# Optimization experiments

Hardware: AMD Instinct MI355X
Metric: run time of the kernel (lower is better)

The kernel has to match this reference:

```python
import jax, jax.numpy as jnp
import numpy as np

GAM1 = 1.0
GAM2 = 1.0
EPS = 0.01


def setup_inputs() -> dict:
    key = jax.random.key(0)
    kx, ky = jax.random.split(key)
    m, p, k = 16384, 512, 10
    X = jax.random.normal(kx, (m, p), dtype=jnp.float32)
    Y = jax.random.randint(ky, (m,), 0, k, dtype=jnp.int64)
    return {"X": X, "Y": Y, "num_classes": k}


def reference(X, Y, num_classes):
    # W: [p, m] (features x samples), as in the torch module (W = X.T)
    W = X.reshape(X.shape[0], -1).T
    p, m = W.shape
    I = jnp.eye(p, dtype=W.dtype)

    # ---- empirical discriminative loss ----
    scalar = p / (m * EPS)
    G = W @ W.T  # [p, p]
    discrimn = jnp.linalg.slogdet(I + GAM1 * scalar * G)[1] / 2.0

    # ---- empirical compressive loss ----
    # Pi[j] is diagonal with the one-hot membership of class j, so
    # W @ Pi[j] @ W.T == (W * mask_j) @ W.T. Build all k masked Grams at once.
    M = jax.nn.one_hot(Y, num_classes, dtype=W.dtype)  # [m, k]
    trPi = M.sum(axis=0) + 1e-8                         # [k] class counts
    # Gk[j] = sum_{i in class j} w_i w_i^T  -> [k, p, p]
    Gk = jnp.einsum('pm,mk,qm->kpq', W, M, W)
    scal = (p / (trPi * EPS))[:, None, None]
    logdets = jnp.linalg.slogdet(I[None] + scal * Gk)[1]  # [k]
    compress = jnp.sum(logdets * trPi / m) / 2.0

    return (discrimn, compress)
```

## Files before the change

kernel.cpp:

```cpp
#include <hip/hip_runtime.h>
#include <math.h>

#define P 512
#define KC 10
#define NB 32
#define EPSV 0.01f
#define TR_ROWS 448
#define XT 17024

typedef __attribute__((ext_vector_type(8))) __bf16 bf16x8;
typedef __attribute__((ext_vector_type(4))) float floatx4;

__global__ __launch_bounds__(256) void sort_k(const int* __restrict__ Y, int* __restrict__ colmap,
                                              int* __restrict__ counts, int* __restrict__ off_pad, int m){
  __shared__ int cnt[KC], offp[KC + 1], cur[KC];
  int tid = threadIdx.x;
  if (tid < KC) cnt[tid] = 0;
  __syncthreads();
  for (int i = tid; i < m; i += 256){
    int y = Y[i];
    if (y >= 0 && y < KC) atomicAdd(&cnt[y], 1);
  }
  __syncthreads();
  if (tid == 0){
    int s = 0;
    for (int j = 0; j < KC; ++j){ offp[j] = s; s += ((cnt[j] + 63) >> 6) << 6; }
    offp[KC] = s;
  }
  __syncthreads();
  if (tid < KC){ cur[tid] = offp[tid]; counts[tid] = cnt[tid]; off_pad[tid] = offp[tid]; }
  if (tid == KC) off_pad[KC] = offp[KC];
  for (int i = tid; i < XT; i += 256) colmap[i] = -1;
  __syncthreads();
  for (int i = tid; i < m; i += 256){
    int y = Y[i];
    if (y >= 0 && y < KC){
      int pos = atomicAdd(&cur[y], 1);
      colmap[pos] = i;
    }
  }
}

__global__ __launch_bounds__(256) void xt_k(const float* __restrict__ X, const int* __restrict__ colmap,
                                            __bf16* __restrict__ Xhi, __bf16* __restrict__ Xlo){
  __shared__ float T[64][65];
  int c0 = blockIdx.x * 64;
  int f0 = blockIdx.y * 64;
  int tid = threadIdx.x;

  int j = tid >> 2;
  int piece = tid & 3;
  int s = colmap[c0 + j];
  if (s >= 0){
    const float* src = X + (long)s * P + f0 + piece * 16;
    #pragma unroll
    for (int q = 0; q < 4; ++q){
      float4 v = *(const float4*)(src + q * 4);
      T[piece * 16 + q * 4 + 0][j] = v.x;
      T[piece * 16 + q * 4 + 1][j] = v.y;
      T[piece * 16 + q * 4 + 2][j] = v.z;
      T[piece * 16 + q * 4 + 3][j] = v.w;
    }
  } else {
    #pragma unroll
    for (int q = 0; q < 16; ++q) T[piece * 16 + q][j] = 0.f;
  }
  __syncthreads();

  int f = tid >> 2;
  int cp = (tid & 3) * 16;
  bf16x8 vh0, vl0, vh1, vl1;
  #pragma unroll
  for (int q = 0; q < 8; ++q){
    float x0 = T[f][cp + q];
    float x1 = T[f][cp + 8 + q];
    __bf16 h0 = (__bf16)x0, h1 = (__bf16)x1;
    vh0[q] = h0; vl0[q] = (__bf16)(x0 - (float)h0);
    vh1[q] = h1; vl1[q] = (__bf16)(x1 - (float)h1);
  }
  long base = (long)(f0 + f) * XT + c0 + cp;
  *(bf16x8*)&Xhi[base]     = vh0;
  *(bf16x8*)&Xhi[base + 8] = vh1;
  *(bf16x8*)&Xlo[base]     = vl0;
  *(bf16x8*)&Xlo[base + 8] = vl1;
}

__global__ __launch_bounds__(256) void gram_mfma(const __bf16* __restrict__ Xhi,
                                                 const __bf16* __restrict__ Xlo,
                                                 const int* __restrict__ counts,
                                                 const int* __restrict__ off_pad,
                                                 float* __restrict__ Gk){
  int cls = blockIdx.y;
  int ta = 0, rem = blockIdx.x;
  while (rem >= ta + 1){ rem -= ta + 1; ++ta; }
  int tb = rem;
  int a0 = ta * 64, b0 = tb * 64;

  int tid  = threadIdx.x;
  int lane = tid & 63;
  int wv   = tid >> 6;
  int wrow = wv >> 1, wcol = wv & 1;
  int fr   = lane & 15;
  int quad = lane >> 4;

  int cs0     = off_pad[cls];
  int nchunks = (counts[cls] + 31) >> 5;

  long arow0 = (long)(a0 + wrow * 32 + fr) * XT;
  long brow0 = (long)(b0 + wcol * 32 + fr) * XT;

  floatx4 acc[2][2];
  #pragma unroll
  for (int i = 0; i < 2; ++i)
    #pragma unroll
    for (int j = 0; j < 2; ++j) acc[i][j] = (floatx4){0.f, 0.f, 0.f, 0.f};

  for (int ch = 0; ch < nchunks; ++ch){
    long co = cs0 + ch * 32 + quad * 8;
    bf16x8 ah[2], al[2], bh[2], bl[2];
    #pragma unroll
    for (int r = 0; r < 2; ++r){
      ah[r] = *(const bf16x8*)&Xhi[arow0 + (long)r * 16 * XT + co];
      al[r] = *(const bf16x8*)&Xlo[arow0 + (long)r * 16 * XT + co];
      bh[r] = *(const bf16x8*)&Xhi[brow0 + (long)r * 16 * XT + co];
      bl[r] = *(const bf16x8*)&Xlo[brow0 + (long)r * 16 * XT + co];
    }
    #pragma unroll
    for (int ri = 0; ri < 2; ++ri)
      #pragma unroll
      for (int rj = 0; rj < 2; ++rj){
        acc[ri][rj] = __builtin_amdgcn_mfma_f32_16x16x32_bf16(al[ri], bh[rj], acc[ri][rj], 0, 0, 0);
        acc[ri][rj] = __builtin_amdgcn_mfma_f32_16x16x32_bf16(ah[ri], bl[rj], acc[ri][rj], 0, 0, 0);
        acc[ri][rj] = __builtin_amdgcn_mfma_f32_16x16x32_bf16(ah[ri], bh[rj], acc[ri][rj], 0, 0, 0);
      }
  }

  float* C = Gk + (long)cls * P * P;
  #pragma unroll
  for (int ri = 0; ri < 2; ++ri){
    int a = a0 + wrow * 32 + ri * 16 + (lane >> 4) * 4;
    #pragma unroll
    for (int rj = 0; rj < 2; ++rj){
      int b = b0 + wcol * 32 + rj * 16 + (lane & 15);
      #pragma unroll
      for (int r = 0; r < 4; ++r)
        C[(long)(a + r) * P + b] = acc[ri][rj][r];
    }
  }
}

__global__ __launch_bounds__(256) void sum10_k(float* __restrict__ Gk){
  long i = (long)blockIdx.x * 256 + threadIdx.x;
  float4 s = {0.f, 0.f, 0.f, 0.f};
  #pragma unroll
  for (int j = 0; j < KC; ++j){
    float4 v = ((const float4*)(Gk + (long)j * P * P))[i];
    s.x += v.x; s.y += v.y; s.z += v.z; s.w += v.w;
  }
  ((float4*)(Gk + (long)KC * P * P))[i] = s;
}

__global__ __launch_bounds__(1024) void chol_mfma(float* __restrict__ Gk,
                                                  const int* __restrict__ counts,
                                                  float* __restrict__ logdets,
                                                  float m_tot){
  __shared__ __bf16 Lhi[TR_ROWS * 32];
  __shared__ __bf16 Llo[TR_ROWS * 32];
  __shared__ float  Ld[NB * 33];
  __shared__ float  Ldr[NB];

  int mat  = blockIdx.x;
  int tid  = threadIdx.x;
  int lane = tid & 63;
  int wv   = tid >> 6;
  float* A = Gk + (long)mat * P * P;
  float sc = (mat < KC) ? ((float)P / (((float)counts[mat] + 1e-8f) * EPSV))
                        : ((float)P / (m_tot * EPSV));
  float logsum = 0.f;

  for (int s = 0; s < 16; ++s){
    int j0 = s * NB;
    int qt = P - j0 - NB;

    if (wv == 0){
      float a[NB];
      if (lane < NB){
        const float* src = A + (long)(j0 + lane) * P + j0;
        #pragma unroll
        for (int u = 0; u < NB; u += 4){
          float4 v = *(const float4*)(src + u);
          a[u] = v.x; a[u+1] = v.y; a[u+2] = v.z; a[u+3] = v.w;
        }
        if (s == 0){
          #pragma unroll
          for (int u = 0; u < NB; ++u) a[u] *= sc;
          a[lane] += 1.0f;
        }
      } else {
        #pragma unroll
        for (int u = 0; u < NB; ++u) a[u] = 0.f;
      }
      #pragma unroll
      for (int jj = 0; jj < NB; ++jj){
        float d = __shfl(a[jj], jj);
        if (lane == 0) logsum += logf(d);
        float inv = 1.0f / d;
        float rs  = rsqrtf(d);
        float w   = a[jj] * inv;
        #pragma unroll
        for (int l = 0; l < NB; ++l){
          if (l > jj){
            float prl = __shfl(a[l], jj);
            a[l] -= w * prl;
          }
        }
        a[jj] *= rs;
      }
      if (lane < NB){
        #pragma unroll
        for (int u = 0; u < NB; ++u) Ld[lane * 33 + u] = a[u];
        Ldr[lane] = 1.0f / a[lane];
      }
    }
    __syncthreads();

    if (qt > 0){
      if (tid < qt){
        float b[NB];
        const float* src = A + (long)(j0 + NB + tid) * P + j0;
        #pragma unroll
        for (int u = 0; u < NB; u += 4){
          float4 v = *(const float4*)(src + u);
          b[u] = v.x; b[u+1] = v.y; b[u+2] = v.z; b[u+3] = v.w;
        }
        if (s == 0){
          #pragma unroll
          for (int u = 0; u < NB; ++u) b[u] *= sc;
        }
        #pragma unroll
        for (int jj = 0; jj < NB; ++jj){
          float acc = b[jj];
          for (int u = 0; u < jj; ++u) acc -= b[u] * Ld[jj * 33 + u];
          b[jj] = acc * Ldr[jj];
        }
        int t = tid;
        #pragma unroll
        for (int c = 0; c < 4; ++c){
          int sw = (t * 4 + (c ^ ((t >> 1) & 3))) * 8;
          bf16x8 vh, vl;
          #pragma unroll
          for (int j = 0; j < 8; ++j){
            float f = b[c * 8 + j];
            __bf16 h = (__bf16)f;
            vh[j] = h;
            vl[j] = (__bf16)(f - (float)h);
          }
          *(bf16x8*)&Lhi[sw] = vh;
          *(bf16x8*)&Llo[sw] = vl;
        }
      }
    }
    __syncthreads();

    if (qt > 0){
      int tt = qt >> 5;
      int T  = tt * (tt + 1) / 2;
      int trail0 = j0 + NB;
      for (int idx = wv; idx < T; idx += 16){
        int ti = 0, rem = idx;
        while (rem >= ti + 1){ rem -= ti + 1; ++ti; }
        int tj = rem;
        int I0 = ti * 32, J0 = tj * 32;
        int c  = lane >> 4;

        bf16x8 ahi[2], alo[2], bhi[2], blo[2];
        #pragma unroll
        for (int h = 0; h < 2; ++h){
          int r1 = I0 + h * 16 + (lane & 15);
          int sw1 = (r1 * 4 + (c ^ ((r1 >> 1) & 3))) * 8;
          ahi[h] = *(const bf16x8*)&Lhi[sw1];
          alo[h] = *(const bf16x8*)&Llo[sw1];
          int r2 = J0 + h * 16 + (lane & 15);
          int sw2 = (r2 * 4 + (c ^ ((r2 >> 1) & 3))) * 8;
          bhi[h] = *(const bf16x8*)&Lhi[sw2];
          blo[h] = *(const bf16x8*)&Llo[sw2];
        }

        #pragma unroll
        for (int hi_ = 0; hi_ < 2; ++hi_){
          #pragma unroll
          for (int hj = 0; hj < 2; ++hj){
            floatx4 acc = {0.f, 0.f, 0.f, 0.f};
            acc = __builtin_amdgcn_mfma_f32_16x16x32_bf16(alo[hi_], bhi[hj], acc, 0, 0, 0);
            acc = __builtin_amdgcn_mfma_f32_16x16x32_bf16(ahi[hi_], blo[hj], acc, 0, 0, 0);
            acc = __builtin_amdgcn_mfma_f32_16x16x32_bf16(ahi[hi_], bhi[hj], acc, 0, 0, 0);
            int grow0 = trail0 + I0 + hi_ * 16 + (lane >> 4) * 4;
            int gcol  = trail0 + J0 + hj  * 16 + (lane & 15);
            #pragma unroll
            for (int r = 0; r < 4; ++r){
              long off = (long)(grow0 + r) * P + gcol;
              float v = A[off];
              if (s == 0) v = sc * v + ((grow0 + r) == gcol ? 1.f : 0.f);
              A[off] = v - acc[r];
            }
          }
        }
      }
    }
    __syncthreads();
  }

  if (tid == 0) logdets[mat] = logsum;
}

__global__ __launch_bounds__(64) void final_k(const float* __restrict__ logdets,
                                              const int* __restrict__ counts,
                                              float* __restrict__ out, float m_tot){
  if (threadIdx.x == 0 && blockIdx.x == 0){
    out[0] = 0.5f * logdets[KC];
    float comp = 0.f;
    for (int j = 0; j < KC; ++j){
      float trPi = (float)counts[j] + 1e-8f;
      comp += logdets[j] * trPi / m_tot;
    }
    out[1] = 0.5f * comp;
  }
}

extern "C" void kernel_launch(void* const* d_in, const int* in_sizes, int n_in,
                              void* d_out, int out_size, void* d_ws, size_t ws_size,
                              hipStream_t stream) {
  (void)n_in; (void)out_size; (void)ws_size;
  const float* X = (const float*)d_in[0];
  const int*   Y = (const int*)d_in[1];
  int m = in_sizes[0] / P;

  float*  Gk      = (float*)d_ws;
  __bf16* Xhi     = (__bf16*)(Gk + 11L * P * P);
  __bf16* Xlo     = Xhi + (long)P * XT;
  int*    colmap  = (int*)(Xlo + (long)P * XT);
  int*    counts  = colmap + XT;
  int*    off_pad = counts + 16;
  float*  logdets = (float*)(off_pad + 17);

  sort_k<<<1, 256, 0, stream>>>(Y, colmap, counts, off_pad, m);

  dim3 xg(XT / 64, 8);
  xt_k<<<xg, 256, 0, stream>>>(X, colmap, Xhi, Xlo);

  dim3 gg(36, KC);
  gram_mfma<<<gg, 256, 0, stream>>>(Xhi, Xlo, counts, off_pad, Gk);

  sum10_k<<<P * P / 1024, 256, 0, stream>>>(Gk);

  chol_mfma<<<KC + 1, 1024, 0, stream>>>(Gk, counts, logdets, (float)m);

  final_k<<<1, 64, 0, stream>>>(logdets, counts, (float*)d_out, (float)m);
}
```

Baseline: 499.3 us.

## Use MFMA with explicit diagonal-block inverse for panel TRSM, fuse final reduction

The panel triangular solve in the blocked Cholesky no longer runs as a serial per-thread forward substitution. Wave 0 now explicitly inverts the 32x32 diagonal factor into shared memory, and all waves compute the panel as a 16-row-tile product with that inverse using split-bf16 MFMA. The log-diagonal sum uses a shuffle reduction, and the separate final kernel is replaced by a last-block-done atomic counter inside the Cholesky kernel. This cuts serial ALU latency in the panel step and removes one launch. In exchange it adds an explicit inverse, which can lose some accuracy, and an extra bf16 rounding of the panel result.

```diff
diff --git a/kernel.cpp b/kernel.cpp
--- a/kernel.cpp
+++ b/kernel.cpp
@@ -12,9 +12,11 @@
 typedef __attribute__((ext_vector_type(4))) float floatx4;
 
 __global__ __launch_bounds__(256) void sort_k(const int* __restrict__ Y, int* __restrict__ colmap,
-                                              int* __restrict__ counts, int* __restrict__ off_pad, int m){
+                                              int* __restrict__ counts, int* __restrict__ off_pad,
+                                              int* __restrict__ done, int m){
   __shared__ int cnt[KC], offp[KC + 1], cur[KC];
   int tid = threadIdx.x;
+  if (tid == 0) *done = 0;
   if (tid < KC) cnt[tid] = 0;
   __syncthreads();
   for (int i = tid; i < m; i += 256){
@@ -163,16 +165,20 @@
 __global__ __launch_bounds__(1024) void chol_mfma(float* __restrict__ Gk,
                                                   const int* __restrict__ counts,
                                                   float* __restrict__ logdets,
+                                                  int* __restrict__ done,
+                                                  float* __restrict__ out,
                                                   float m_tot){
   __shared__ __bf16 Lhi[TR_ROWS * 32];
   __shared__ __bf16 Llo[TR_ROWS * 32];
   __shared__ float  Ld[NB * 33];
   __shared__ float  Ldr[NB];
+  __shared__ float  Minv[NB * 36];
 
   int mat  = blockIdx.x;
   int tid  = threadIdx.x;
   int lane = tid & 63;
   int wv   = tid >> 6;
+  int quad = lane >> 4;
   float* A = Gk + (long)mat * P * P;
   float sc = (mat < KC) ? ((float)P / (((float)counts[mat] + 1e-8f) * EPSV))
                         : ((float)P / (m_tot * EPSV));
@@ -184,6 +190,7 @@
 
     if (wv == 0){
       float a[NB];
+      float myp = 1.f;
       if (lane < NB){
         const float* src = A + (long)(j0 + lane) * P + j0;
         #pragma unroll
@@ -203,60 +210,86 @@
       #pragma unroll
       for (int jj = 0; jj < NB; ++jj){
         float d = __shfl(a[jj], jj);
-        if (lane == 0) logsum += logf(d);
+        if (lane == jj) myp = d;
         float inv = 1.0f / d;
         float rs  = rsqrtf(d);
         float w   = a[jj] * inv;
         #pragma unroll
-        for (int l = 0; l < NB; ++l){
-          if (l > jj){
-            float prl = __shfl(a[l], jj);
-            a[l] -= w * prl;
-          }
-        }
-        a[jj] *= rs;
+        for (int l = jj + 1; l < NB; ++l){
+          float prl = __shfl(a[l], jj);
+          if (lane > jj) a[l] -= w * prl;
+        }
+        if (lane >= jj) a[jj] *= rs;
       }
       if (lane < NB){
         #pragma unroll
         for (int u = 0; u < NB; ++u) Ld[lane * 33 + u] = a[u];
         Ldr[lane] = 1.0f / a[lane];
       }
+      if (lane < NB){
+        float x[NB];
+        #pragma unroll
+        for (int r2 = 0; r2 < NB; ++r2){
+          float acc2 = (r2 == lane) ? 1.f : 0.f;
+          #pragma unroll
+          for (int u = 0; u < r2; ++u)
+            acc2 -= Ld[r2 * 33 + u] * x[u];
+          x[r2] = acc2 * Ldr[r2];
+        }
+        #pragma unroll
+        for (int r2 = 0; r2 < NB; ++r2) Minv[r2 * 36 + lane] = x[r2];
+      }
+      float lp = (lane < NB) ? logf(myp) : 0.f;
+      #pragma unroll
+      for (int off = 16; off >= 1; off >>= 1) lp += __shfl_xor(lp, off);
+      if (tid == 0) logsum += lp;
     }
     __syncthreads();
 
     if (qt > 0){
-      if (tid < qt){
-        float b[NB];
-        const float* src = A + (long)(j0 + NB + tid) * P + j0;
-        #pragma unroll
-        for (int u = 0; u < NB; u += 4){
-          float4 v = *(const float4*)(src + u);
-          b[u] = v.x; b[u+1] = v.y; b[u+2] = v.z; b[u+3] = v.w;
-        }
+      int nrt = qt >> 4;
+      for (int rt = wv; rt < nrt; rt += 16){
+        int grow = j0 + NB + rt * 16 + (lane & 15);
+        const float* src = A + (long)grow * P + j0 + quad * 8;
+        float4 v0 = *(const float4*)src;
+        float4 v1 = *(const float4*)(src + 4);
+        float av[8] = {v0.x, v0.y, v0.z, v0.w, v1.x, v1.y, v1.z, v1.w};
         if (s == 0){
           #pragma unroll
-          for (int u = 0; u < NB; ++u) b[u] *= sc;
-        }
-        #pragma unroll
-        for (int jj = 0; jj < NB; ++jj){
-          float acc = b[jj];
-          for (int u = 0; u < jj; ++u) acc -= b[u] * Ld[jj * 33 + u];
-          b[jj] = acc * Ldr[jj];
-        }
-        int t = tid;
-        #pragma unroll
-        for (int c = 0; c < 4; ++c){
-          int sw = (t * 4 + (c ^ ((t >> 1) & 3))) * 8;
-          bf16x8 vh, vl;
-          #pragma unroll
-          for (int j = 0; j < 8; ++j){
-            float f = b[c * 8 + j];
-            __bf16 h = (__bf16)f;
-            vh[j] = h;
-            vl[j] = (__bf16)(f - (float)h);
+          for (int u = 0; u < 8; ++u) av[u] *= sc;
+        }
+        bf16x8 ah, al;
+        #pragma unroll
+        for (int u = 0; u < 8; ++u){
+          __bf16 h = (__bf16)av[u];
+          ah[u] = h; al[u] = (__bf16)(av[u] - (float)h);
+        }
+        #pragma unroll
+        for (int h2 = 0; h2 < 2; ++h2){
+          const float* mp = &Minv[(h2 * 16 + (lane & 15)) * 36 + quad * 8];
+          float4 m0 = *(const float4*)mp;
+          float4 m1 = *(const float4*)(mp + 4);
+          float mv[8] = {m0.x, m0.y, m0.z, m0.w, m1.x, m1.y, m1.z, m1.w};
+          bf16x8 bh, bl;
+          #pragma unroll
+          for (int u = 0; u < 8; ++u){
+            __bf16 h = (__bf16)mv[u];
+            bh[u] = h; bl[u] = (__bf16)(mv[u] - (float)h);
           }
-          *(bf16x8*)&Lhi[sw] = vh;
-          *(bf16x8*)&Llo[sw] = vl;
+          floatx4 acc = {0.f, 0.f, 0.f, 0.f};
+          acc = __builtin_amdgcn_mfma_f32_16x16x32_bf16(al, bh, acc, 0, 0, 0);
+          acc = __builtin_amdgcn_mfma_f32_16x16x32_bf16(ah, bl, acc, 0, 0, 0);
+          acc = __builtin_amdgcn_mfma_f32_16x16x32_bf16(ah, bh, acc, 0, 0, 0);
+          #pragma unroll
+          for (int r = 0; r < 4; ++r){
+            int t   = rt * 16 + quad * 4 + r;
+            int col = h2 * 16 + (lane & 15);
+            float y = acc[r];
+            __bf16 hh = (__bf16)y;
+            int ad = (t * 4 + ((col >> 3) ^ ((t >> 1) & 3))) * 8 + (col & 7);
+            Lhi[ad] = hh;
+            Llo[ad] = (__bf16)(y - (float)hh);
+          }
         }
       }
     }
@@ -271,7 +304,7 @@
         while (rem >= ti + 1){ rem -= ti + 1; ++ti; }
         int tj = rem;
         int I0 = ti * 32, J0 = tj * 32;
-        int c  = lane >> 4;
+        int c  = quad;
 
         bf16x8 ahi[2], alo[2], bhi[2], blo[2];
         #pragma unroll
@@ -310,20 +343,22 @@
     __syncthreads();
   }
 
-  if (tid == 0) logdets[mat] = logsum;
-}
-
-__global__ __launch_bounds__(64) void final_k(const float* __restrict__ logdets,
-                                              const int* __restrict__ counts,
-                                              float* __restrict__ out, float m_tot){
-  if (threadIdx.x == 0 && blockIdx.x == 0){
-    out[0] = 0.5f * logdets[KC];
-    float comp = 0.f;
-    for (int j = 0; j < KC; ++j){
-      float trPi = (float)counts[j] + 1e-8f;
-      comp += logdets[j] * trPi / m_tot;
-    }
-    out[1] = 0.5f * comp;
+  if (tid == 0){
+    __hip_atomic_store(&logdets[mat], logsum, __ATOMIC_RELEASE, __HIP_MEMORY_SCOPE_AGENT);
+    int old = __hip_atomic_fetch_add(done, 1, __ATOMIC_ACQ_REL, __HIP_MEMORY_SCOPE_AGENT);
+    if (old == KC){
+      float ld[KC + 1];
+      #pragma unroll
+      for (int j = 0; j <= KC; ++j)
+        ld[j] = __hip_atomic_load(&logdets[j], __ATOMIC_ACQUIRE, __HIP_MEMORY_SCOPE_AGENT);
+      out[0] = 0.5f * ld[KC];
+      float comp = 0.f;
+      for (int j = 0; j < KC; ++j){
+        float trPi = (float)counts[j] + 1e-8f;
+        comp += ld[j] * trPi / m_tot;
+      }
+      out[1] = 0.5f * comp;
+    }
   }
 }
 
@@ -341,9 +376,10 @@
   int*    colmap  = (int*)(Xlo + (long)P * XT);
   int*    counts  = colmap + XT;
   int*    off_pad = counts + 16;
-  float*  logdets = (float*)(off_pad + 17);
-
-  sort_k<<<1, 256, 0, stream>>>(Y, colmap, counts, off_pad, m);
+  int*    done    = off_pad + 17;
+  float*  logdets = (float*)(done + 1);
+
+  sort_k<<<1, 256, 0, stream>>>(Y, colmap, counts, off_pad, done, m);
 
   dim3 xg(XT / 64, 8);
   xt_k<<<xg, 256, 0, stream>>>(X, colmap, Xhi, Xlo);
@@ -353,7 +389,5 @@
 
   sum10_k<<<P * P / 1024, 256, 0, stream>>>(Gk);
 
-  chol_mfma<<<KC + 1, 1024, 0, stream>>>(Gk, counts, logdets, (float)m);
-
-  final_k<<<1, 64, 0, stream>>>(logdets, counts, (float*)d_out, (float)m);
-}
+  chol_mfma<<<KC + 1, 1024, 0, stream>>>(Gk, counts, logdets, done, (float*)d_out, (float)m);
+}
```

Result: slower. 613.3 us (+22.8%).
